# Kernel optimization log

Hardware: AMD Instinct MI355X
Metric: run time of the kernel (lower is better)

## Reference

```python
import jax, jax.numpy as jnp
import numpy as np
from jax import lax

N_NODES = 50000
N_EDGES = 1_600_000
B, T = 4, 12
GCN_H, TCN_H, OUT_LEN = 32, 32, 1


def setup_inputs() -> dict:
    key = jax.random.key(0)
    ks = jax.random.split(key, 8)
    return {
        "x_seq": jax.random.normal(ks[0], (B, T, N_NODES), jnp.float32),
        "edge_index": jax.random.randint(ks[1], (2, N_EDGES), 0, N_NODES, jnp.int64),
        "edge_weight": jax.random.uniform(ks[2], (N_EDGES,), jnp.float32),
        "gcn_w": jax.random.normal(ks[3], (1, GCN_H), jnp.float32) * 0.5,
        "gcn_b": jnp.zeros((GCN_H,), jnp.float32),
        "conv_w": jax.random.normal(ks[4], (TCN_H, GCN_H, 3), jnp.float32) * 0.1,
        "conv_b": jnp.zeros((TCN_H,), jnp.float32),
        "lin_w": jax.random.normal(ks[5], (TCN_H, OUT_LEN), jnp.float32) * 0.1,
        "lin_b": jnp.zeros((OUT_LEN,), jnp.float32),
    }


def _gcn_agg(x, src, dst, norm, n):
    msgs = x[:, src] * norm[None, :]                      # [BT, E+N]
    return jax.vmap(lambda m: jax.ops.segment_sum(m, dst, num_segments=n))(msgs)


def reference(x_seq, edge_index, edge_weight, gcn_w, gcn_b, conv_w, conv_b, lin_w, lin_b):
    b, t, n = x_seq.shape
    src, dst = edge_index[0], edge_index[1]
    # GCN normalization with self-loops (fill_value=1.0), as PyG GCNConv
    loops = jnp.arange(n)
    src_f = jnp.concatenate([src, loops])
    dst_f = jnp.concatenate([dst, loops])
    ew_f = jnp.concatenate([edge_weight, jnp.ones((n,), x_seq.dtype)])
    deg = jax.ops.segment_sum(ew_f, dst_f, num_segments=n)
    dinv = jnp.where(deg > 0, deg ** -0.5, 0.0)
    norm = dinv[src_f] * ew_f * dinv[dst_f]               # [E+N]
    # GCN is linear: A_hat (X W) == (A_hat X) W ; X has 1 channel -> aggregate scalars
    x = x_seq.reshape(b * t, n)                           # [BT, N]
    agg = _gcn_agg(x, src_f, dst_f, norm, n)              # [BT, N]
    h = agg[..., None] * gcn_w[0][None, None, :] + gcn_b  # [BT, N, H]
    # temporal conv over T: reshape to [B*N, H, T]
    h = h.reshape(b, t, n, GCN_H).transpose(0, 2, 3, 1).reshape(b * n, GCN_H, t)
    y = lax.conv_general_dilated(h, conv_w, window_strides=(1,), padding=[(1, 1)],
                                 dimension_numbers=("NCH", "OIH", "NCH"))
    y = jax.nn.relu(y + conv_b[None, :, None])            # [B*N, H, T]
    pooled = y.mean(axis=-1)                              # [B*N, H]
    out = pooled @ lin_w + lin_b                          # [B*N, out_len]
    return out.reshape(b, n, -1).transpose(0, 2, 1)       # [B, out_len, N]
```

## Files before the change

kernel.cpp:

```cpp
#include <hip/hip_runtime.h>
#include <math.h>

#define N_NODES 50000
#define N_EDGES 1600000
#define BT 48
#define CAP 80
#define BINSZ 64
#define NBINS 782
#define ECHUNK 4096
#define SBLOCK 1024

__global__ __launch_bounds__(1024) void init_k(int* __restrict__ sc) {
  int i = threadIdx.x;
  if (i < NBINS) sc[i] = 0;
}

__global__ __launch_bounds__(SBLOCK) void stage_k(const int* __restrict__ ei,
                                                  const float* __restrict__ ew,
                                                  int* __restrict__ stage_cnt,
                                                  int2* __restrict__ staged,
                                                  int scap) {
  __shared__ int hist[NBINS];
  __shared__ int ptr[NBINS];
  int t = threadIdx.x;
  for (int b = t; b < NBINS; b += SBLOCK) hist[b] = 0;
  __syncthreads();

  int e0 = blockIdx.x * ECHUNK;
  int ne = min(ECHUNK, N_EDGES - e0);

  for (int k = t; k < ne; k += SBLOCK) {
    int d = ei[N_EDGES + e0 + k];
    atomicAdd(&hist[d >> 6], 1);
  }
  __syncthreads();
  for (int b = t; b < NBINS; b += SBLOCK) {
    int h = hist[b];
    ptr[b] = h ? atomicAdd(&stage_cnt[b], h) : 0;
  }
  __syncthreads();
  for (int k = t; k < ne; k += SBLOCK) {
    int e = e0 + k;
    int s = ei[e];
    int d = ei[N_EDGES + e];
    float w = ew[e];
    int b = d >> 6;
    int p = atomicAdd(&ptr[b], 1);
    if (p < scap)
      staged[(size_t)b * scap + p] = make_int2(s | ((d & 63) << 16), __float_as_int(w));
  }
}

__global__ __launch_bounds__(256) void build_k(const int2* __restrict__ staged,
                                               const int* __restrict__ stage_cnt,
                                               int2* __restrict__ ell,
                                               int* __restrict__ cnt,
                                               float* __restrict__ dinv,
                                               int scap) {
  __shared__ int2 rows[BINSZ][CAP];
  __shared__ int rcnt[BINSZ];
  int t = threadIdx.x, b = blockIdx.x;
  if (t < BINSZ) rcnt[t] = 0;
  __syncthreads();

  int ne = min(stage_cnt[b], scap);
  const int2* sp = staged + (size_t)b * scap;
  for (int k = t; k < ne; k += 256) {
    int2 m = sp[k];
    int dloc = (m.x >> 16) & 63;
    int src  = m.x & 0xffff;
    int slot = atomicAdd(&rcnt[dloc], 1);
    if (slot < CAP) rows[dloc][slot] = make_int2(src, m.y);
  }
  __syncthreads();

  int base = b * BINSZ;
  if (t < BINSZ) {
    int n = base + t;
    if (n < N_NODES) {
      int c = min(rcnt[t], CAP);
      float s = 0.0f;
      for (int i = 0; i < c; ++i) s += __int_as_float(rows[t][i].y);
      cnt[n] = c;
      dinv[n] = 1.0f / sqrtf(1.0f + s);
    }
  }
  __syncthreads();

  int r = t & 63, st = t >> 6;
  int n = base + r;
  if (n < N_NODES) {
    int c = min(rcnt[r], CAP);
    int2* dst = ell + (size_t)n * CAP;
    for (int i = st; i < c; i += 4) dst[i] = rows[r][i];
  }
}

__global__ __launch_bounds__(256) void transpose_k(const float* __restrict__ x,
                                                   const float* __restrict__ dinv,
                                                   float* __restrict__ xs) {
  int n = blockIdx.x * 256 + threadIdx.x;
  if (n >= N_NODES) return;
  float dn = dinv[n];
  float tmp[BT];
#pragma unroll
  for (int bt = 0; bt < BT; ++bt) tmp[bt] = dn * x[(size_t)bt * N_NODES + n];
  float4* dst = (float4*)(xs + (size_t)n * BT);
#pragma unroll
  for (int j = 0; j < BT / 4; ++j)
    dst[j] = make_float4(tmp[4 * j], tmp[4 * j + 1], tmp[4 * j + 2], tmp[4 * j + 3]);
}

__global__ __launch_bounds__(256) void spmm_k(const float* __restrict__ xs,
                                              const int2* __restrict__ ell,
                                              const int* __restrict__ cnt,
                                              const float* __restrict__ dinv,
                                              float* __restrict__ agg) {
  int lane = threadIdx.x & 63;
  int n = (blockIdx.x * 256 + threadIdx.x) >> 6;
  if (n >= N_NODES) return;
  int col = (lane < BT) ? lane : (BT - 1);
  const int2* pp = ell + (size_t)n * CAP;
  int c = __builtin_amdgcn_readfirstlane(cnt[n]);
  int2 m = pp[lane];
  float acc = 0.0f;
  int cm = (c < 64) ? c : 64;

  int e = 0;
  for (; e + 8 <= cm; e += 8) {
    int   s0 = __builtin_amdgcn_readlane(m.x, e + 0);
    int   s1 = __builtin_amdgcn_readlane(m.x, e + 1);
    int   s2 = __builtin_amdgcn_readlane(m.x, e + 2);
    int   s3 = __builtin_amdgcn_readlane(m.x, e + 3);
    int   s4 = __builtin_amdgcn_readlane(m.x, e + 4);
    int   s5 = __builtin_amdgcn_readlane(m.x, e + 5);
    int   s6 = __builtin_amdgcn_readlane(m.x, e + 6);
    int   s7 = __builtin_amdgcn_readlane(m.x, e + 7);
    float w0 = __int_as_float(__builtin_amdgcn_readlane(m.y, e + 0));
    float w1 = __int_as_float(__builtin_amdgcn_readlane(m.y, e + 1));
    float w2 = __int_as_float(__builtin_amdgcn_readlane(m.y, e + 2));
    float w3 = __int_as_float(__builtin_amdgcn_readlane(m.y, e + 3));
    float w4 = __int_as_float(__builtin_amdgcn_readlane(m.y, e + 4));
    float w5 = __int_as_float(__builtin_amdgcn_readlane(m.y, e + 5));
    float w6 = __int_as_float(__builtin_amdgcn_readlane(m.y, e + 6));
    float w7 = __int_as_float(__builtin_amdgcn_readlane(m.y, e + 7));
    float x0 = xs[(size_t)s0 * BT + col];
    float x1 = xs[(size_t)s1 * BT + col];
    float x2 = xs[(size_t)s2 * BT + col];
    float x3 = xs[(size_t)s3 * BT + col];
    float x4 = xs[(size_t)s4 * BT + col];
    float x5 = xs[(size_t)s5 * BT + col];
    float x6 = xs[(size_t)s6 * BT + col];
    float x7 = xs[(size_t)s7 * BT + col];
    acc = fmaf(w0, x0, acc); acc = fmaf(w1, x1, acc);
    acc = fmaf(w2, x2, acc); acc = fmaf(w3, x3, acc);
    acc = fmaf(w4, x4, acc); acc = fmaf(w5, x5, acc);
    acc = fmaf(w6, x6, acc); acc = fmaf(w7, x7, acc);
  }
  for (; e < cm; ++e) {
    int   s = __builtin_amdgcn_readlane(m.x, e);
    float w = __int_as_float(__builtin_amdgcn_readlane(m.y, e));
    acc = fmaf(w, xs[(size_t)s * BT + col], acc);
  }
  for (; e < c; ++e) {
    int2 q = pp[e];
    int   s = __builtin_amdgcn_readfirstlane(q.x);
    float w = __int_as_float(__builtin_amdgcn_readfirstlane(q.y));
    acc = fmaf(w, xs[(size_t)s * BT + col], acc);
  }

  if (lane < BT) {
    float dn = dinv[n];
    float r = dn * (acc + xs[(size_t)n * BT + col]);
    __builtin_nontemporal_store(r, &agg[(size_t)n * BT + col]);
  }
}

__global__ void coeff_k(const float* __restrict__ conv_w, const float* __restrict__ gcn_w,
                        const float* __restrict__ gcn_b, float* __restrict__ wv,
                        float* __restrict__ wb) {
  int idx = threadIdx.x;
  if (idx >= 96) return;
  int co = idx / 3, k = idx % 3;
  float sv = 0.0f, sb = 0.0f;
  for (int ci = 0; ci < 32; ++ci) {
    float w = conv_w[co * 96 + ci * 3 + k];
    sv += w * gcn_w[ci];
    sb += w * gcn_b[ci];
  }
  wv[idx] = sv;
  wb[idx] = sb;
}

__global__ __launch_bounds__(256) void epi_k(const float* __restrict__ agg,
                                             const float* __restrict__ wv,
                                             const float* __restrict__ wb,
                                             const float* __restrict__ conv_b,
                                             const float* __restrict__ lin_w,
                                             const float* __restrict__ lin_b,
                                             float* __restrict__ out) {
  __shared__ float s_wv[96], s_wb[96], s_cb[32], s_lw[32], s_lb;
  int tid = threadIdx.x;
  if (tid < 96) { s_wv[tid] = wv[tid]; s_wb[tid] = wb[tid]; }
  if (tid < 32) { s_cb[tid] = conv_b[tid]; s_lw[tid] = lin_w[tid]; }
  if (tid == 0) s_lb = lin_b[0];
  __syncthreads();

  int n = blockIdx.x * 256 + tid;
  if (n >= N_NODES) return;
  const float4* ap = (const float4*)(agg + (size_t)n * BT);

#pragma unroll
  for (int b = 0; b < 4; ++b) {
    float4 q0 = ap[b * 3], q1 = ap[b * 3 + 1], q2 = ap[b * 3 + 2];
    float a[14];
    a[0] = 0.0f; a[13] = 0.0f;
    a[1] = q0.x; a[2] = q0.y; a[3] = q0.z; a[4] = q0.w;
    a[5] = q1.x; a[6] = q1.y; a[7] = q1.z; a[8] = q1.w;
    a[9] = q2.x; a[10] = q2.y; a[11] = q2.z; a[12] = q2.w;

    float acc = 0.0f;
    for (int co = 0; co < 32; ++co) {
      float w0 = s_wv[3 * co], w1 = s_wv[3 * co + 1], w2 = s_wv[3 * co + 2];
      float b0 = s_wb[3 * co], b1 = s_wb[3 * co + 1], b2 = s_wb[3 * co + 2];
      float base = s_cb[co] + b1;
      float lw = s_lw[co];
      float sr = 0.0f;
#pragma unroll
      for (int t = 0; t < 12; ++t) {
        float v = base + w0 * a[t] + w1 * a[t + 1] + w2 * a[t + 2];
        if (t > 0)  v += b0;
        if (t < 11) v += b2;
        sr += fmaxf(v, 0.0f);
      }
      acc = fmaf(lw, sr, acc);
    }
    out[b * N_NODES + n] = s_lb + acc * (1.0f / 12.0f);
  }
}

extern "C" void kernel_launch(void* const* d_in, const int* in_sizes, int n_in,
                              void* d_out, int out_size, void* d_ws, size_t ws_size,
                              hipStream_t stream) {
  const float* x_seq  = (const float*)d_in[0];
  const int*   ei     = (const int*)d_in[1];
  const float* ew     = (const float*)d_in[2];
  const float* gcn_w  = (const float*)d_in[3];
  const float* gcn_b  = (const float*)d_in[4];
  const float* conv_w = (const float*)d_in[5];
  const float* conv_b = (const float*)d_in[6];
  const float* lin_w  = (const float*)d_in[7];
  const float* lin_b  = (const float*)d_in[8];
  float* out = (float*)d_out;

  char* ws = (char*)d_ws;
  size_t off = 0;
  auto alloc = [&](size_t bytes) -> void* {
    void* p = ws + off;
    off += (bytes + 511) & ~(size_t)511;
    return p;
  };
  float* dinv = (float*)alloc((size_t)N_NODES * 4);
  int*   cnt  = (int*)alloc((size_t)N_NODES * 4);
  float* wv   = (float*)alloc(96 * 4);
  float* wb   = (float*)alloc(96 * 4);
  int*   sc   = (int*)alloc((size_t)NBINS * 4);
  int2*  ell  = (int2*)alloc((size_t)N_NODES * CAP * 8);

  size_t remain = (ws_size > off) ? (ws_size - off) : 0;
  int scap = (int)(remain / ((size_t)NBINS * 8));
  if (scap > 4096) scap = 4096;
  if (scap < 3072) scap = 3072;
  int2* staged = (int2*)alloc((size_t)NBINS * scap * 8);
  float* xs  = (float*)staged;
  float* agg = (float*)((char*)staged + (size_t)N_NODES * BT * 4);

  const int nblk = (N_NODES + 255) / 256;
  const int sblk = (N_EDGES + ECHUNK - 1) / ECHUNK;
  const int wblk = (N_NODES * 64 + 255) / 256;

  hipLaunchKernelGGL(init_k, dim3(1), dim3(1024), 0, stream, sc);
  hipLaunchKernelGGL(stage_k, dim3(sblk), dim3(SBLOCK), 0, stream, ei, ew, sc, staged, scap);
  hipLaunchKernelGGL(build_k, dim3(NBINS), dim3(256), 0, stream, staged, sc, ell, cnt, dinv, scap);
  hipLaunchKernelGGL(transpose_k, dim3(nblk), dim3(256), 0, stream, x_seq, dinv, xs);
  hipLaunchKernelGGL(spmm_k, dim3(wblk), dim3(256), 0, stream, xs, ell, cnt, dinv, agg);
  hipLaunchKernelGGL(coeff_k, dim3(1), dim3(128), 0, stream, conv_w, gcn_w, gcn_b, wv, wb);
  hipLaunchKernelGGL(epi_k, dim3(nblk), dim3(256), 0, stream, agg, wv, wb, conv_b, lin_w, lin_b, out);
}
```

Before: 212.1 us.

## Fuse SpMM with temporal-conv epilogue and store scaled features in fp16

Merges the sparse aggregation and the conv/ReLU/mean/linear epilogue into one kernel. Each wave stages its node's 48 aggregated values in shared memory, then 16-lane groups split the output channels and reduce them with xor shuffles. This removes the intermediate agg buffer write and read. The pre-scaled node features are stored as fp16, which halves the random-gather traffic but adds rounding error. The gather loop is unrolled to 16, and the init kernel is replaced by hipMemsetAsync.

```diff
diff --git a/kernel.cpp b/kernel.cpp
--- a/kernel.cpp
+++ b/kernel.cpp
@@ -1,4 +1,5 @@
 #include <hip/hip_runtime.h>
+#include <hip/hip_fp16.h>
 #include <math.h>
 
 #define N_NODES 50000
@@ -9,11 +10,6 @@
 #define NBINS 782
 #define ECHUNK 4096
 #define SBLOCK 1024
-
-__global__ __launch_bounds__(1024) void init_k(int* __restrict__ sc) {
-  int i = threadIdx.x;
-  if (i < NBINS) sc[i] = 0;
-}
 
 __global__ __launch_bounds__(SBLOCK) void stage_k(const int* __restrict__ ei,
                                                   const float* __restrict__ ew,
@@ -98,82 +94,21 @@
 
 __global__ __launch_bounds__(256) void transpose_k(const float* __restrict__ x,
                                                    const float* __restrict__ dinv,
-                                                   float* __restrict__ xs) {
+                                                   __half* __restrict__ xs) {
   int n = blockIdx.x * 256 + threadIdx.x;
   if (n >= N_NODES) return;
   float dn = dinv[n];
-  float tmp[BT];
-#pragma unroll
-  for (int bt = 0; bt < BT; ++bt) tmp[bt] = dn * x[(size_t)bt * N_NODES + n];
+  __half2 h2[BT / 2];
+#pragma unroll
+  for (int j = 0; j < BT / 2; ++j) {
+    float a = dn * x[(size_t)(2 * j) * N_NODES + n];
+    float b = dn * x[(size_t)(2 * j + 1) * N_NODES + n];
+    h2[j] = __floats2half2_rn(a, b);
+  }
   float4* dst = (float4*)(xs + (size_t)n * BT);
-#pragma unroll
-  for (int j = 0; j < BT / 4; ++j)
-    dst[j] = make_float4(tmp[4 * j], tmp[4 * j + 1], tmp[4 * j + 2], tmp[4 * j + 3]);
-}
-
-__global__ __launch_bounds__(256) void spmm_k(const float* __restrict__ xs,
-                                              const int2* __restrict__ ell,
-                                              const int* __restrict__ cnt,
-                                              const float* __restrict__ dinv,
-                                              float* __restrict__ agg) {
-  int lane = threadIdx.x & 63;
-  int n = (blockIdx.x * 256 + threadIdx.x) >> 6;
-  if (n >= N_NODES) return;
-  int col = (lane < BT) ? lane : (BT - 1);
-  const int2* pp = ell + (size_t)n * CAP;
-  int c = __builtin_amdgcn_readfirstlane(cnt[n]);
-  int2 m = pp[lane];
-  float acc = 0.0f;
-  int cm = (c < 64) ? c : 64;
-
-  int e = 0;
-  for (; e + 8 <= cm; e += 8) {
-    int   s0 = __builtin_amdgcn_readlane(m.x, e + 0);
-    int   s1 = __builtin_amdgcn_readlane(m.x, e + 1);
-    int   s2 = __builtin_amdgcn_readlane(m.x, e + 2);
-    int   s3 = __builtin_amdgcn_readlane(m.x, e + 3);
-    int   s4 = __builtin_amdgcn_readlane(m.x, e + 4);
-    int   s5 = __builtin_amdgcn_readlane(m.x, e + 5);
-    int   s6 = __builtin_amdgcn_readlane(m.x, e + 6);
-    int   s7 = __builtin_amdgcn_readlane(m.x, e + 7);
-    float w0 = __int_as_float(__builtin_amdgcn_readlane(m.y, e + 0));
-    float w1 = __int_as_float(__builtin_amdgcn_readlane(m.y, e + 1));
-    float w2 = __int_as_float(__builtin_amdgcn_readlane(m.y, e + 2));
-    float w3 = __int_as_float(__builtin_amdgcn_readlane(m.y, e + 3));
-    float w4 = __int_as_float(__builtin_amdgcn_readlane(m.y, e + 4));
-    float w5 = __int_as_float(__builtin_amdgcn_readlane(m.y, e + 5));
-    float w6 = __int_as_float(__builtin_amdgcn_readlane(m.y, e + 6));
-    float w7 = __int_as_float(__builtin_amdgcn_readlane(m.y, e + 7));
-    float x0 = xs[(size_t)s0 * BT + col];
-    float x1 = xs[(size_t)s1 * BT + col];
-    float x2 = xs[(size_t)s2 * BT + col];
-    float x3 = xs[(size_t)s3 * BT + col];
-    float x4 = xs[(size_t)s4 * BT + col];
-    float x5 = xs[(size_t)s5 * BT + col];
-    float x6 = xs[(size_t)s6 * BT + col];
-    float x7 = xs[(size_t)s7 * BT + col];
-    acc = fmaf(w0, x0, acc); acc = fmaf(w1, x1, acc);
-    acc = fmaf(w2, x2, acc); acc = fmaf(w3, x3, acc);
-    acc = fmaf(w4, x4, acc); acc = fmaf(w5, x5, acc);
-    acc = fmaf(w6, x6, acc); acc = fmaf(w7, x7, acc);
-  }
-  for (; e < cm; ++e) {
-    int   s = __builtin_amdgcn_readlane(m.x, e);
-    float w = __int_as_float(__builtin_amdgcn_readlane(m.y, e));
-    acc = fmaf(w, xs[(size_t)s * BT + col], acc);
-  }
-  for (; e < c; ++e) {
-    int2 q = pp[e];
-    int   s = __builtin_amdgcn_readfirstlane(q.x);
-    float w = __int_as_float(__builtin_amdgcn_readfirstlane(q.y));
-    acc = fmaf(w, xs[(size_t)s * BT + col], acc);
-  }
-
-  if (lane < BT) {
-    float dn = dinv[n];
-    float r = dn * (acc + xs[(size_t)n * BT + col]);
-    __builtin_nontemporal_store(r, &agg[(size_t)n * BT + col]);
-  }
+  const float4* srcp = (const float4*)h2;
+#pragma unroll
+  for (int j = 0; j < 6; ++j) dst[j] = srcp[j];
 }
 
 __global__ void coeff_k(const float* __restrict__ conv_w, const float* __restrict__ gcn_w,
@@ -192,51 +127,104 @@
   wb[idx] = sb;
 }
 
-__global__ __launch_bounds__(256) void epi_k(const float* __restrict__ agg,
-                                             const float* __restrict__ wv,
-                                             const float* __restrict__ wb,
-                                             const float* __restrict__ conv_b,
-                                             const float* __restrict__ lin_w,
-                                             const float* __restrict__ lin_b,
-                                             float* __restrict__ out) {
-  __shared__ float s_wv[96], s_wb[96], s_cb[32], s_lw[32], s_lb;
+__global__ __launch_bounds__(256) void spmm_epi_k(const __half* __restrict__ xs,
+                                                  const int2* __restrict__ ell,
+                                                  const int* __restrict__ cnt,
+                                                  const float* __restrict__ dinv,
+                                                  const float* __restrict__ wv,
+                                                  const float* __restrict__ wb,
+                                                  const float* __restrict__ conv_b,
+                                                  const float* __restrict__ lin_w,
+                                                  const float* __restrict__ lin_b,
+                                                  float* __restrict__ out) {
+  __shared__ float s_wv[96], s_wb[96], s_cb[32], s_lw[32];
+  __shared__ float s_lb;
+  __shared__ float sAgg[4][BT];
   int tid = threadIdx.x;
   if (tid < 96) { s_wv[tid] = wv[tid]; s_wb[tid] = wb[tid]; }
   if (tid < 32) { s_cb[tid] = conv_b[tid]; s_lw[tid] = lin_w[tid]; }
   if (tid == 0) s_lb = lin_b[0];
   __syncthreads();
 
-  int n = blockIdx.x * 256 + tid;
-  if (n >= N_NODES) return;
-  const float4* ap = (const float4*)(agg + (size_t)n * BT);
-
-#pragma unroll
-  for (int b = 0; b < 4; ++b) {
-    float4 q0 = ap[b * 3], q1 = ap[b * 3 + 1], q2 = ap[b * 3 + 2];
-    float a[14];
-    a[0] = 0.0f; a[13] = 0.0f;
-    a[1] = q0.x; a[2] = q0.y; a[3] = q0.z; a[4] = q0.w;
-    a[5] = q1.x; a[6] = q1.y; a[7] = q1.z; a[8] = q1.w;
-    a[9] = q2.x; a[10] = q2.y; a[11] = q2.z; a[12] = q2.w;
-
-    float acc = 0.0f;
-    for (int co = 0; co < 32; ++co) {
-      float w0 = s_wv[3 * co], w1 = s_wv[3 * co + 1], w2 = s_wv[3 * co + 2];
-      float b0 = s_wb[3 * co], b1 = s_wb[3 * co + 1], b2 = s_wb[3 * co + 2];
-      float base = s_cb[co] + b1;
-      float lw = s_lw[co];
-      float sr = 0.0f;
-#pragma unroll
-      for (int t = 0; t < 12; ++t) {
-        float v = base + w0 * a[t] + w1 * a[t + 1] + w2 * a[t + 2];
-        if (t > 0)  v += b0;
-        if (t < 11) v += b2;
-        sr += fmaxf(v, 0.0f);
-      }
-      acc = fmaf(lw, sr, acc);
-    }
-    out[b * N_NODES + n] = s_lb + acc * (1.0f / 12.0f);
-  }
+  int lane = tid & 63;
+  int wid  = tid >> 6;
+  int n = (blockIdx.x * 256 + tid) >> 6;
+  int col = (lane < BT) ? lane : (BT - 1);
+  const int2* pp = ell + (size_t)n * CAP;
+  int c = __builtin_amdgcn_readfirstlane(cnt[n]);
+  int2 m = pp[lane];
+  float acc = 0.0f;
+  int cm = (c < 64) ? c : 64;
+
+  int e = 0;
+  for (; e + 16 <= cm; e += 16) {
+    float xv[16], wgt[16];
+#pragma unroll
+    for (int k = 0; k < 16; ++k) {
+      int s  = __builtin_amdgcn_readlane(m.x, e + k);
+      wgt[k] = __int_as_float(__builtin_amdgcn_readlane(m.y, e + k));
+      xv[k]  = __half2float(xs[(size_t)s * BT + col]);
+    }
+#pragma unroll
+    for (int k = 0; k < 16; ++k) acc = fmaf(wgt[k], xv[k], acc);
+  }
+  for (; e + 8 <= cm; e += 8) {
+    float xv[8], wgt[8];
+#pragma unroll
+    for (int k = 0; k < 8; ++k) {
+      int s  = __builtin_amdgcn_readlane(m.x, e + k);
+      wgt[k] = __int_as_float(__builtin_amdgcn_readlane(m.y, e + k));
+      xv[k]  = __half2float(xs[(size_t)s * BT + col]);
+    }
+#pragma unroll
+    for (int k = 0; k < 8; ++k) acc = fmaf(wgt[k], xv[k], acc);
+  }
+  for (; e < cm; ++e) {
+    int   s = __builtin_amdgcn_readlane(m.x, e);
+    float w = __int_as_float(__builtin_amdgcn_readlane(m.y, e));
+    acc = fmaf(w, __half2float(xs[(size_t)s * BT + col]), acc);
+  }
+  for (; e < c; ++e) {
+    int2 q = pp[e];
+    int   s = __builtin_amdgcn_readfirstlane(q.x);
+    float w = __int_as_float(__builtin_amdgcn_readfirstlane(q.y));
+    acc = fmaf(w, __half2float(xs[(size_t)s * BT + col]), acc);
+  }
+
+  float dn = dinv[n];
+  float xsn = __half2float(xs[(size_t)n * BT + col]);
+  if (lane < BT) sAgg[wid][col] = dn * (acc + xsn);
+
+  int b = lane >> 4;
+  float a[14];
+  a[0] = 0.0f; a[13] = 0.0f;
+#pragma unroll
+  for (int t = 0; t < 12; ++t) a[t + 1] = sAgg[wid][b * 12 + t];
+
+  float part = 0.0f;
+#pragma unroll
+  for (int cc = 0; cc < 2; ++cc) {
+    int co = (lane & 15) + cc * 16;
+    float w0 = s_wv[3 * co], w1 = s_wv[3 * co + 1], w2 = s_wv[3 * co + 2];
+    float b0 = s_wb[3 * co], b1 = s_wb[3 * co + 1], b2 = s_wb[3 * co + 2];
+    float base = s_cb[co] + b1;
+    float lw = s_lw[co];
+    float sr = 0.0f;
+#pragma unroll
+    for (int t = 0; t < 12; ++t) {
+      float v = base + w0 * a[t] + w1 * a[t + 1] + w2 * a[t + 2];
+      if (t > 0)  v += b0;
+      if (t < 11) v += b2;
+      sr += fmaxf(v, 0.0f);
+    }
+    part = fmaf(lw, sr, part);
+  }
+  part += __shfl_xor(part, 1, 64);
+  part += __shfl_xor(part, 2, 64);
+  part += __shfl_xor(part, 4, 64);
+  part += __shfl_xor(part, 8, 64);
+  if ((lane & 15) == 0)
+    out[(size_t)b * N_NODES + n] = s_lb + part * (1.0f / 12.0f);
 }
 
 extern "C" void kernel_launch(void* const* d_in, const int* in_sizes, int n_in,
@@ -272,18 +260,17 @@
   if (scap > 4096) scap = 4096;
   if (scap < 3072) scap = 3072;
   int2* staged = (int2*)alloc((size_t)NBINS * scap * 8);
-  float* xs  = (float*)staged;
-  float* agg = (float*)((char*)staged + (size_t)N_NODES * BT * 4);
+  __half* xs = (__half*)staged;
 
   const int nblk = (N_NODES + 255) / 256;
   const int sblk = (N_EDGES + ECHUNK - 1) / ECHUNK;
-  const int wblk = (N_NODES * 64 + 255) / 256;
-
-  hipLaunchKernelGGL(init_k, dim3(1), dim3(1024), 0, stream, sc);
+  const int wblk = (N_NODES * 64) / 256;
+
+  hipMemsetAsync(sc, 0, (size_t)NBINS * 4, stream);
   hipLaunchKernelGGL(stage_k, dim3(sblk), dim3(SBLOCK), 0, stream, ei, ew, sc, staged, scap);
   hipLaunchKernelGGL(build_k, dim3(NBINS), dim3(256), 0, stream, staged, sc, ell, cnt, dinv, scap);
   hipLaunchKernelGGL(transpose_k, dim3(nblk), dim3(256), 0, stream, x_seq, dinv, xs);
-  hipLaunchKernelGGL(spmm_k, dim3(wblk), dim3(256), 0, stream, xs, ell, cnt, dinv, agg);
   hipLaunchKernelGGL(coeff_k, dim3(1), dim3(128), 0, stream, conv_w, gcn_w, gcn_b, wv, wb);
-  hipLaunchKernelGGL(epi_k, dim3(nblk), dim3(256), 0, stream, agg, wv, wb, conv_b, lin_w, lin_b, out);
-}
+  hipLaunchKernelGGL(spmm_epi_k, dim3(wblk), dim3(256), 0, stream,
+                     xs, ell, cnt, dinv, wv, wb, conv_b, lin_w, lin_b, out);
+}
```

Measured after the change: 188.7 us. -11.0%, faster.
